# Kernel optimization log

Measured on AMD Instinct MI355X. Metric: run time of the kernel, lower is better.

Reference implementation:

```python
import jax, jax.numpy as jnp
import numpy as np

B, S, DIM, H = 8, 4096, 1024, 16
HD = DIM // H
SCALE = HD ** -0.5


def setup_inputs() -> dict:
    key = jax.random.key(0)
    k1, k2, k3 = jax.random.split(key, 3)
    x = jax.random.normal(k1, (B, S, DIM), dtype=jnp.float32)
    # xavier_uniform-ish scales (exact init irrelevant for correctness baseline)
    Wqkv = jax.random.normal(k2, (DIM, 3 * DIM), dtype=jnp.float32) * (2.0 / (DIM + DIM)) ** 0.5
    bqkv = jnp.zeros((3 * DIM,), dtype=jnp.float32)
    Wproj = jax.random.normal(k3, (DIM, DIM), dtype=jnp.float32) * (2.0 / (DIM + DIM)) ** 0.5
    bproj = jnp.zeros((DIM,), dtype=jnp.float32)
    return {"x": x, "Wqkv": Wqkv, "bqkv": bqkv, "Wproj": Wproj, "bproj": bproj}


def reference(x, Wqkv, bqkv, Wproj, bproj):
    b, s, _ = x.shape
    qkv = x @ Wqkv + bqkv                                  # [b, s, 3*dim]
    qkv = qkv.reshape(b, s, 3, H, HD)
    q, k, v = [jnp.transpose(qkv[:, :, i], (0, 2, 1, 3)) for i in range(3)]  # each [b, h, s, hd]
    q = jax.nn.softmax(q, axis=-2) * SCALE                 # softmax over seqlen
    k = jax.nn.softmax(k, axis=-1)                         # softmax over head_dim
    # original computes (k @ v^T)^T @ q; associativity gives v @ (k^T @ q), O(n*d^2)
    A = jnp.einsum("bhtd,bhte->bhde", k, q)                # [b, h, hd, hd]
    out = jnp.einsum("bhsd,bhde->bhse", v, A)              # [b, h, s, hd]
    out = jnp.transpose(out, (0, 2, 1, 3)).reshape(b, s, DIM)
    return out @ Wproj + bproj
```

## Files before the change

kernel.cpp:

```cpp
#include <hip/hip_runtime.h>
#include <hip/hip_bf16.h>

typedef short s16x8 __attribute__((ext_vector_type(8)));
typedef float f32x4 __attribute__((ext_vector_type(4)));
typedef unsigned int u32x4 __attribute__((ext_vector_type(4)));
typedef unsigned int u32x2 __attribute__((ext_vector_type(2)));

__device__ __forceinline__ float b2f(unsigned short u) {
  unsigned int v = ((unsigned int)u) << 16;
  return __builtin_bit_cast(float, v);
}
__device__ __forceinline__ unsigned short f2b(float f) {
  __hip_bfloat16 h = __float2bfloat16(f);
  return __builtin_bit_cast(unsigned short, h);
}

__global__ __launch_bounds__(256) void cast_x_kernel(const float* __restrict__ x,
                                                     unsigned short* __restrict__ xb) {
  int i = (blockIdx.x * 256 + threadIdx.x) * 4;
  f32x4 v = *(const f32x4*)(x + i);
  u32x2 o;
  o[0] = (unsigned)f2b(v[0]) | ((unsigned)f2b(v[1]) << 16);
  o[1] = (unsigned)f2b(v[2]) | ((unsigned)f2b(v[3]) << 16);
  *(u32x2*)(xb + i) = o;
}

__global__ __launch_bounds__(256) void wtrans_kernel(const float* __restrict__ W,
                                                     unsigned short* __restrict__ Wt,
                                                     int K, int N) {
  __shared__ float tile[64][65];
  int n0 = blockIdx.x * 64, k0 = blockIdx.y * 64;
  int tx = threadIdx.x & 63, ty = threadIdx.x >> 6;
  #pragma unroll
  for (int i = ty; i < 64; i += 4) tile[i][tx] = W[(long)(k0 + i) * N + n0 + tx];
  __syncthreads();
  #pragma unroll
  for (int i = ty; i < 64; i += 4) Wt[(long)(n0 + i) * K + k0 + tx] = f2b(tile[tx][i]);
}

template<bool BF16OUT>
__global__ __launch_bounds__(256) void gemm_bt_kernel(
    const unsigned short* __restrict__ A, int lda,
    const unsigned short* __restrict__ Bt0, int ldb,
    const float* __restrict__ bias,
    void* __restrict__ Cv, int N, int K,
    int rows_per_batch, long bstride) {
  __shared__ unsigned short a_lds[128 * 40];
  __shared__ unsigned short b_lds[128 * 40];
  const int tid = threadIdx.x;
  const int lane = tid & 63, wid = tid >> 6;
  const int m0 = blockIdx.y * 128, n0 = blockIdx.x * 128;
  const int wm = (wid >> 1) * 64, wn = (wid & 1) * 64;
  const int fm = lane & 15, fq = lane >> 4;

  const unsigned short* Bt = Bt0;
  if (rows_per_batch) Bt += (long)(m0 / rows_per_batch) * bstride;

  f32x4 acc[4][4] = {};

  const int r0 = tid >> 2;
  const int c0 = (tid & 3) * 8;
  const unsigned short* Aptr0 = A + (long)(m0 + r0) * lda + c0;
  const unsigned short* Aptr1 = Aptr0 + (long)64 * lda;
  const unsigned short* Bptr0 = Bt + (long)(n0 + r0) * ldb + c0;
  const unsigned short* Bptr1 = Bptr0 + (long)64 * ldb;
  unsigned short* a_st0 = &a_lds[r0 * 40 + c0];
  unsigned short* a_st1 = &a_lds[(r0 + 64) * 40 + c0];
  unsigned short* b_st0 = &b_lds[r0 * 40 + c0];
  unsigned short* b_st1 = &b_lds[(r0 + 64) * 40 + c0];

  for (int k0 = 0; k0 < K; k0 += 32) {
    u32x4 va0 = *(const u32x4*)(Aptr0 + k0);
    u32x4 va1 = *(const u32x4*)(Aptr1 + k0);
    u32x4 vb0 = *(const u32x4*)(Bptr0 + k0);
    u32x4 vb1 = *(const u32x4*)(Bptr1 + k0);
    __syncthreads();
    *(u32x4*)a_st0 = va0;
    *(u32x4*)a_st1 = va1;
    *(u32x4*)b_st0 = vb0;
    *(u32x4*)b_st1 = vb1;
    __syncthreads();
    s16x8 af[4], bfr[4];
    #pragma unroll
    for (int i = 0; i < 4; i++) {
      af[i]  = *(const s16x8*)&a_lds[(wm + i * 16 + fm) * 40 + fq * 8];
      bfr[i] = *(const s16x8*)&b_lds[(wn + i * 16 + fm) * 40 + fq * 8];
    }
    #pragma unroll
    for (int mi = 0; mi < 4; mi++)
      #pragma unroll
      for (int ni = 0; ni < 4; ni++)
        acc[mi][ni] = __builtin_amdgcn_mfma_f32_16x16x32_bf16(af[mi], bfr[ni], acc[mi][ni], 0, 0, 0);
  }

  #pragma unroll
  for (int ni = 0; ni < 4; ni++) {
    const int col = n0 + wn + ni * 16 + fm;
    const float bv = bias[col];
    #pragma unroll
    for (int mi = 0; mi < 4; mi++) {
      #pragma unroll
      for (int r = 0; r < 4; r++) {
        const long row = m0 + wm + mi * 16 + fq * 4 + r;
        const float v = acc[mi][ni][r] + bv;
        if (BF16OUT) ((unsigned short*)Cv)[row * N + col] = f2b(v);
        else         ((float*)Cv)[row * N + col] = v;
      }
    }
  }
}

__global__ __launch_bounds__(256) void apass_kernel(
    const unsigned short* __restrict__ qkv,
    float* __restrict__ Ap,
    float* __restrict__ Dp) {
  __shared__ unsigned short qs_lds[32 * 68];
  __shared__ unsigned short ks_lds[32 * 68];
  __shared__ float dled[64];
  const int tid = threadIdx.x;
  const int chunk = blockIdx.x, g = blockIdx.y;
  const int b = g >> 4, h = g & 15;
  const int w = tid >> 6, lane = tid & 63;
  const int fm = lane & 15, fq = lane >> 4;
  const int tl = tid >> 3;
  const int c0 = (tid & 7) * 8;

  if (tid < 64) dled[tid] = 0.f;

  const long row0 = (long)(b * 4096 + chunk * 1024 + tl);
  const unsigned short* qptr = qkv + row0 * 3072 + h * 64 + c0;
  const unsigned short* kptr = qptr + 1024;

  f32x4 acc[4] = {};
  float dacc[8] = {};

  unsigned short* qst = &qs_lds[tl * 68 + c0];
  unsigned short* kst = &ks_lds[tl * 68 + c0];

  for (int ks = 0; ks < 32; ks++) {
    const long roff = (long)(ks * 32) * 3072;
    u32x4 qv = *(const u32x4*)(qptr + roff);
    u32x4 kv = *(const u32x4*)(kptr + roff);
    float qe[8], ke[8];
    #pragma unroll
    for (int i = 0; i < 4; i++) {
      qe[2*i]   = __expf(b2f((unsigned short)(qv[i] & 0xffffu)));
      qe[2*i+1] = __expf(b2f((unsigned short)(qv[i] >> 16)));
      ke[2*i]   = __expf(b2f((unsigned short)(kv[i] & 0xffffu)));
      ke[2*i+1] = __expf(b2f((unsigned short)(kv[i] >> 16)));
    }
    float p = 0.f;
    #pragma unroll
    for (int i = 0; i < 8; i++) p += ke[i];
    p += __shfl_xor(p, 1);
    p += __shfl_xor(p, 2);
    p += __shfl_xor(p, 4);
    const float kinv = 1.0f / p;
    unsigned int qpk[4], kpk[4];
    #pragma unroll
    for (int i = 0; i < 4; i++) {
      qpk[i] = (unsigned)f2b(qe[2*i] * kinv) | ((unsigned)f2b(qe[2*i+1] * kinv) << 16);
      kpk[i] = (unsigned)f2b(ke[2*i]) | ((unsigned)f2b(ke[2*i+1]) << 16);
      dacc[2*i]   += qe[2*i];
      dacc[2*i+1] += qe[2*i+1];
    }
    __syncthreads();
    u32x2 t0, t1;
    t0[0] = qpk[0]; t0[1] = qpk[1]; t1[0] = qpk[2]; t1[1] = qpk[3];
    *(u32x2*)qst = t0; *(u32x2*)(qst + 4) = t1;
    t0[0] = kpk[0]; t0[1] = kpk[1]; t1[0] = kpk[2]; t1[1] = kpk[3];
    *(u32x2*)kst = t0; *(u32x2*)(kst + 4) = t1;
    __syncthreads();
    s16x8 af;
    #pragma unroll
    for (int j = 0; j < 8; j++)
      af[j] = (short)qs_lds[(fq * 8 + j) * 68 + (w * 16 + fm)];
    #pragma unroll
    for (int ni = 0; ni < 4; ni++) {
      s16x8 bfr;
      #pragma unroll
      for (int j = 0; j < 8; j++)
        bfr[j] = (short)ks_lds[(fq * 8 + j) * 68 + (ni * 16 + fm)];
      acc[ni] = __builtin_amdgcn_mfma_f32_16x16x32_bf16(af, bfr, acc[ni], 0, 0, 0);
    }
  }
  float* ap = Ap + (long)(chunk * 128 + g) * 4096;
  #pragma unroll
  for (int ni = 0; ni < 4; ni++)
    #pragma unroll
    for (int r = 0; r < 4; r++)
      ap[(w * 16 + fq * 4 + r) * 64 + ni * 16 + fm] = acc[ni][r];
  #pragma unroll
  for (int i = 0; i < 8; i++) atomicAdd(&dled[c0 + i], dacc[i]);
  __syncthreads();
  if (tid < 64) Dp[(chunk * 8 + b) * 1024 + h * 64 + tid] = dled[tid];
}

__global__ __launch_bounds__(256) void mmake_kernel(
    const float* __restrict__ Ap,
    const float* __restrict__ Dp,
    const float* __restrict__ Wproj,
    unsigned short* __restrict__ Mt) {
  __shared__ float At[4096];
  __shared__ float Wp[4096];
  const int tid = threadIdx.x;
  const int n0 = blockIdx.x * 64;
  const int g = blockIdx.y;
  const int b = g >> 4, h = g & 15;
  #pragma unroll
  for (int j = 0; j < 16; j++) {
    int lin = tid + 256 * j;
    int e = lin >> 6, n = lin & 63;
    float s = 0.f, den = 0.f;
    #pragma unroll
    for (int c = 0; c < 4; c++) {
      s   += Ap[(long)(c * 128 + g) * 4096 + lin];
      den += Dp[(c * 8 + b) * 1024 + h * 64 + e];
    }
    At[lin] = 0.125f * s / den;
    Wp[lin] = Wproj[(long)(h * 64 + e) * 1024 + n0 + n];
  }
  __syncthreads();
  const int d = tid & 63, ng = tid >> 6;
  #pragma unroll
  for (int nn = 0; nn < 16; nn++) {
    const int n = ng * 16 + nn;
    float s = 0.f;
    #pragma unroll
    for (int e = 0; e < 64; e++)
      s = fmaf(At[e * 64 + d], Wp[e * 64 + n], s);
    Mt[((long)b << 20) + (long)(n0 + n) * 1024 + h * 64 + d] = f2b(s);
  }
}

extern "C" void kernel_launch(void* const* d_in, const int* in_sizes, int n_in,
                              void* d_out, int out_size, void* d_ws, size_t ws_size,
                              hipStream_t stream) {
  const float* x     = (const float*)d_in[0];
  const float* Wqkv  = (const float*)d_in[1];
  const float* bqkv  = (const float*)d_in[2];
  const float* Wproj = (const float*)d_in[3];
  const float* bproj = (const float*)d_in[4];
  float* out = (float*)d_out;

  char* ws = (char*)d_ws;
  unsigned short* xb  = (unsigned short*)(ws + 0);
  unsigned short* wqt = (unsigned short*)(ws + 67108864);
  unsigned short* qkv = (unsigned short*)(ws + 73400320);
  float*          ap  = (float*)        (ws + 274726912);
  float*          dp  = (float*)        (ws + 283115520);
  unsigned short* mt  = (unsigned short*)(ws + 283246592);

  cast_x_kernel<<<dim3(32768), dim3(256), 0, stream>>>(x, xb);
  wtrans_kernel<<<dim3(48, 16), dim3(256), 0, stream>>>(Wqkv, wqt, 1024, 3072);
  gemm_bt_kernel<true><<<dim3(24, 256), dim3(256), 0, stream>>>(
      xb, 1024, wqt, 1024, bqkv, (void*)qkv, 3072, 1024, 0, 0);
  apass_kernel<<<dim3(4, 128), dim3(256), 0, stream>>>(qkv, ap, dp);
  mmake_kernel<<<dim3(16, 128), dim3(256), 0, stream>>>(ap, dp, Wproj, mt);
  gemm_bt_kernel<false><<<dim3(8, 256), dim3(256), 0, stream>>>(
      qkv + 2048, 3072, mt, 1024, bproj, (void*)out, 1024, 1024, 4096, 1048576);
}
```

Baseline: 810.0 us.

## Use direct global-to-LDS loads with swizzle in GEMM; transpose apass LDS staging

The GEMM main loop now fills shared memory with global_load_lds (16-byte direct async copies) into an unpadded, XOR-swizzled layout instead of staging through registers, and the fragment reads use the matching swizzle. The apass kernel stores q and k transposed into shared memory so that MFMA fragments can be read as two 4-element vector loads instead of eight scalar loads. The mmake kernel caches the At column in registers for its inner product. The aim is to cut VGPR staging and LDS bank conflicts, at the cost of tying correctness to the swizzle and LDS-address mapping of the async load.

```diff
diff --git a/kernel.cpp b/kernel.cpp
--- a/kernel.cpp
+++ b/kernel.cpp
@@ -2,6 +2,7 @@
 #include <hip/hip_bf16.h>
 
 typedef short s16x8 __attribute__((ext_vector_type(8)));
+typedef short s16x4 __attribute__((ext_vector_type(4)));
 typedef float f32x4 __attribute__((ext_vector_type(4)));
 typedef unsigned int u32x4 __attribute__((ext_vector_type(4)));
 typedef unsigned int u32x2 __attribute__((ext_vector_type(2)));
@@ -13,6 +14,11 @@
 __device__ __forceinline__ unsigned short f2b(float f) {
   __hip_bfloat16 h = __float2bfloat16(f);
   return __builtin_bit_cast(unsigned short, h);
+}
+__device__ __forceinline__ void async_ld16(const unsigned short* g, unsigned short* l) {
+  __builtin_amdgcn_global_load_lds(
+      (const __attribute__((address_space(1))) void*)g,
+      (__attribute__((address_space(3))) void*)l, 16, 0, 0);
 }
 
 __global__ __launch_bounds__(256) void cast_x_kernel(const float* __restrict__ x,
@@ -45,8 +51,8 @@
     const float* __restrict__ bias,
     void* __restrict__ Cv, int N, int K,
     int rows_per_batch, long bstride) {
-  __shared__ unsigned short a_lds[128 * 40];
-  __shared__ unsigned short b_lds[128 * 40];
+  __shared__ unsigned short a_lds[128 * 32];
+  __shared__ unsigned short b_lds[128 * 32];
   const int tid = threadIdx.x;
   const int lane = tid & 63, wid = tid >> 6;
   const int m0 = blockIdx.y * 128, n0 = blockIdx.x * 128;
@@ -58,33 +64,34 @@
 
   f32x4 acc[4][4] = {};
 
-  const int r0 = tid >> 2;
-  const int c0 = (tid & 3) * 8;
-  const unsigned short* Aptr0 = A + (long)(m0 + r0) * lda + c0;
-  const unsigned short* Aptr1 = Aptr0 + (long)64 * lda;
-  const unsigned short* Bptr0 = Bt + (long)(n0 + r0) * ldb + c0;
-  const unsigned short* Bptr1 = Bptr0 + (long)64 * ldb;
-  unsigned short* a_st0 = &a_lds[r0 * 40 + c0];
-  unsigned short* a_st1 = &a_lds[(r0 + 64) * 40 + c0];
-  unsigned short* b_st0 = &b_lds[r0 * 40 + c0];
-  unsigned short* b_st1 = &b_lds[(r0 + 64) * 40 + c0];
+  const unsigned short* gA[2];
+  const unsigned short* gB[2];
+  unsigned short* lA[2];
+  unsigned short* lB[2];
+  #pragma unroll
+  for (int j = 0; j < 2; j++) {
+    const int C = (wid * 2 + j) * 64 + lane;
+    const int r = C >> 2, cp = C & 3;
+    const int cg = cp ^ ((r >> 1) & 3);
+    gA[j] = A + (long)(m0 + r) * lda + cg * 8;
+    gB[j] = Bt + (long)(n0 + r) * ldb + cg * 8;
+    lA[j] = a_lds + (wid * 2 + j) * 512;
+    lB[j] = b_lds + (wid * 2 + j) * 512;
+  }
+  const int swa = (fq ^ ((fm >> 1) & 3)) * 8;
 
   for (int k0 = 0; k0 < K; k0 += 32) {
-    u32x4 va0 = *(const u32x4*)(Aptr0 + k0);
-    u32x4 va1 = *(const u32x4*)(Aptr1 + k0);
-    u32x4 vb0 = *(const u32x4*)(Bptr0 + k0);
-    u32x4 vb1 = *(const u32x4*)(Bptr1 + k0);
-    __syncthreads();
-    *(u32x4*)a_st0 = va0;
-    *(u32x4*)a_st1 = va1;
-    *(u32x4*)b_st0 = vb0;
-    *(u32x4*)b_st1 = vb1;
+    __syncthreads();
+    async_ld16(gA[0] + k0, lA[0]);
+    async_ld16(gA[1] + k0, lA[1]);
+    async_ld16(gB[0] + k0, lB[0]);
+    async_ld16(gB[1] + k0, lB[1]);
     __syncthreads();
     s16x8 af[4], bfr[4];
     #pragma unroll
     for (int i = 0; i < 4; i++) {
-      af[i]  = *(const s16x8*)&a_lds[(wm + i * 16 + fm) * 40 + fq * 8];
-      bfr[i] = *(const s16x8*)&b_lds[(wn + i * 16 + fm) * 40 + fq * 8];
+      af[i]  = *(const s16x8*)&a_lds[(wm + i * 16 + fm) * 32 + swa];
+      bfr[i] = *(const s16x8*)&b_lds[(wn + i * 16 + fm) * 32 + swa];
     }
     #pragma unroll
     for (int mi = 0; mi < 4; mi++)
@@ -114,8 +121,8 @@
     const unsigned short* __restrict__ qkv,
     float* __restrict__ Ap,
     float* __restrict__ Dp) {
-  __shared__ unsigned short qs_lds[32 * 68];
-  __shared__ unsigned short ks_lds[32 * 68];
+  __shared__ unsigned short qT[64 * 36 + 8];
+  __shared__ unsigned short kT[64 * 36 + 8];
   __shared__ float dled[64];
   const int tid = threadIdx.x;
   const int chunk = blockIdx.x, g = blockIdx.y;
@@ -134,9 +141,6 @@
   f32x4 acc[4] = {};
   float dacc[8] = {};
 
-  unsigned short* qst = &qs_lds[tl * 68 + c0];
-  unsigned short* kst = &ks_lds[tl * 68 + c0];
-
   for (int ks = 0; ks < 32; ks++) {
     const long roff = (long)(ks * 32) * 3072;
     u32x4 qv = *(const u32x4*)(qptr + roff);
@@ -156,31 +160,25 @@
     p += __shfl_xor(p, 2);
     p += __shfl_xor(p, 4);
     const float kinv = 1.0f / p;
-    unsigned int qpk[4], kpk[4];
-    #pragma unroll
-    for (int i = 0; i < 4; i++) {
-      qpk[i] = (unsigned)f2b(qe[2*i] * kinv) | ((unsigned)f2b(qe[2*i+1] * kinv) << 16);
-      kpk[i] = (unsigned)f2b(ke[2*i]) | ((unsigned)f2b(ke[2*i+1]) << 16);
-      dacc[2*i]   += qe[2*i];
-      dacc[2*i+1] += qe[2*i+1];
-    }
-    __syncthreads();
-    u32x2 t0, t1;
-    t0[0] = qpk[0]; t0[1] = qpk[1]; t1[0] = qpk[2]; t1[1] = qpk[3];
-    *(u32x2*)qst = t0; *(u32x2*)(qst + 4) = t1;
-    t0[0] = kpk[0]; t0[1] = kpk[1]; t1[0] = kpk[2]; t1[1] = kpk[3];
-    *(u32x2*)kst = t0; *(u32x2*)(kst + 4) = t1;
-    __syncthreads();
-    s16x8 af;
-    #pragma unroll
-    for (int j = 0; j < 8; j++)
-      af[j] = (short)qs_lds[(fq * 8 + j) * 68 + (w * 16 + fm)];
+    #pragma unroll
+    for (int i = 0; i < 8; i++) dacc[i] += qe[i];
+    __syncthreads();
+    #pragma unroll
+    for (int i = 0; i < 8; i++) {
+      qT[(c0 + i) * 36 + tl] = f2b(qe[i] * kinv);
+      kT[(c0 + i) * 36 + tl] = f2b(ke[i]);
+    }
+    __syncthreads();
+    const int aoff = (w * 16 + fm) * 36 + fq * 8;
+    s16x4 alo = *(const s16x4*)&qT[aoff];
+    s16x4 ahi = *(const s16x4*)&qT[aoff + 4];
+    s16x8 af = {alo[0], alo[1], alo[2], alo[3], ahi[0], ahi[1], ahi[2], ahi[3]};
     #pragma unroll
     for (int ni = 0; ni < 4; ni++) {
-      s16x8 bfr;
-      #pragma unroll
-      for (int j = 0; j < 8; j++)
-        bfr[j] = (short)ks_lds[(fq * 8 + j) * 68 + (ni * 16 + fm)];
+      const int boff = (ni * 16 + fm) * 36 + fq * 8;
+      s16x4 blo = *(const s16x4*)&kT[boff];
+      s16x4 bhi = *(const s16x4*)&kT[boff + 4];
+      s16x8 bfr = {blo[0], blo[1], blo[2], blo[3], bhi[0], bhi[1], bhi[2], bhi[3]};
       acc[ni] = __builtin_amdgcn_mfma_f32_16x16x32_bf16(af, bfr, acc[ni], 0, 0, 0);
     }
   }
@@ -222,13 +220,16 @@
   }
   __syncthreads();
   const int d = tid & 63, ng = tid >> 6;
+  float a_reg[64];
+  #pragma unroll
+  for (int e = 0; e < 64; e++) a_reg[e] = At[e * 64 + d];
   #pragma unroll
   for (int nn = 0; nn < 16; nn++) {
     const int n = ng * 16 + nn;
     float s = 0.f;
     #pragma unroll
     for (int e = 0; e < 64; e++)
-      s = fmaf(At[e * 64 + d], Wp[e * 64 + n], s);
+      s = fmaf(a_reg[e], Wp[e * 64 + n], s);
     Mt[((long)b << 20) + (long)(n0 + n) * 1024 + h * 64 + d] = f2b(s);
   }
 }
```

After: 718.8 us. 11.3% less time.
